# Performance work log

Measured on AMD Instinct MI355X. Metric: run time of the kernel, lower is better.

Reference implementation:

```python
import jax, jax.numpy as jnp
import numpy as np

B, L, K, S, D, H, C = 32, 256, 50, 16, 128, 4, 128
V, NN, NU, NS = 50000, 100000, 50000, 5000


def mha(q, k, v, in_w, in_b, out_w, out_b, n_heads):
    # PyTorch nn.MultiheadAttention (batch_first, eval mode) semantics.
    d = q.shape[-1]
    hd = d // n_heads
    wq, wk, wv = jnp.split(in_w, 3, axis=0)
    bq, bk, bv = jnp.split(in_b, 3)
    def heads(t):
        return t.reshape(t.shape[:-1] + (n_heads, hd))
    qh = heads(q @ wq.T + bq)
    kh = heads(k @ wk.T + bk)
    vh = heads(v @ wv.T + bv)
    scores = jnp.einsum('...qhd,...khd->...hqk', qh, kh) / jnp.sqrt(jnp.asarray(hd, q.dtype))
    attn = jax.nn.softmax(scores, axis=-1)
    o = jnp.einsum('...hqk,...khd->...qhd', attn, vh)
    o = o.reshape(o.shape[:-2] + (d,))
    return o @ out_w.T + out_b


def conv1d(x, w, b):
    # x: [B, D, L], w: [Cout, D, k]
    y = jax.lax.conv_general_dilated(x, w, (1,), 'VALID', dimension_numbers=('NCH', 'OIH', 'NCH'))
    return y + b[None, :, None]


def meta_path_module(paths, gru_wih, gru_whh, gru_bih, gru_bhh, in_w, in_b, out_w, out_b, ln_g, ln_b):
    # paths: [B, S, T, D] -> [B, D]
    b, s, t, d = paths.shape
    x = paths.reshape(b * s, t, d)
    def step(h, xt):
        gi = xt @ gru_wih.T + gru_bih
        gh = h @ gru_whh.T + gru_bhh
        ir, iz, inn = jnp.split(gi, 3, axis=-1)
        hr, hz, hn = jnp.split(gh, 3, axis=-1)
        r = jax.nn.sigmoid(ir + hr)
        z = jax.nn.sigmoid(iz + hz)
        n = jnp.tanh(inn + r * hn)
        return (1.0 - z) * n + z * h, None
    h0 = jnp.zeros((b * s, d), paths.dtype)
    h, _ = jax.lax.scan(step, h0, jnp.swapaxes(x, 0, 1))
    enc = h.reshape(b, s, d)
    attn = mha(enc, enc, enc, in_w, in_b, out_w, out_b, H)
    y = enc + attn
    mu = jnp.mean(y, -1, keepdims=True)
    var = jnp.var(y, -1, keepdims=True)
    y = (y - mu) / jnp.sqrt(var + 1e-5) * ln_g + ln_b
    return jnp.mean(y, axis=1)


def _forward(word_table, news_table, user_table, source_table,
             wa_in_w, wa_in_b, wa_out_w, wa_out_b,
             conv_w3, conv_b3, conv_w4, conv_b4, conv_w5, conv_b5, fc_w, fc_b,
             nsn_gru_wih, nsn_gru_whh, nsn_gru_bih, nsn_gru_bhh,
             nsn_in_w, nsn_in_b, nsn_out_w, nsn_out_b, nsn_ln_g, nsn_ln_b,
             nun_gru_wih, nun_gru_whh, nun_gru_bih, nun_gru_bhh,
             nun_in_w, nun_in_b, nun_out_w, nun_out_b, nun_ln_g, nun_ln_b,
             mp_w1, mp_b1, mp_w2, mp_b2, cls_w1, cls_b1, cls_w2, cls_b2,
             news_ids, news_word_indices, word_ctx_ids, nsn_src, nsn_end, nun_usr, nun_end):
    # --- fine-grained word embeds: per-token query attending over context news ---
    base = word_table[news_word_indices]              # [B, L, D]
    ctx = news_table[word_ctx_ids]                    # [B, L, K, D] (dominant gather)
    q = base[:, :, None, :]                           # [B, L, 1, D]
    fine = mha(q, ctx, ctx, wa_in_w, wa_in_b, wa_out_w, wa_out_b, H)[:, :, 0, :]
    pad = (news_word_indices == 0)[..., None]
    doc = jnp.where(pad, jnp.zeros((), base.dtype), fine)   # padding_idx=0 -> zeros
    # --- coarse CNN encoder ---
    x = jnp.swapaxes(doc, 1, 2)                       # [B, D, L]
    pooled = [jnp.max(jax.nn.relu(conv1d(x, w, b)), axis=2)
              for w, b in ((conv_w3, conv_b3), (conv_w4, conv_b4), (conv_w5, conv_b5))]
    semantic = jnp.concatenate(pooled, axis=1) @ fc_w.T + fc_b   # [B, D]
    # --- meta-path interaction ---
    start = jnp.broadcast_to(news_table[news_ids][:, None, :], (B, S, D))
    nsn_paths = jnp.stack([start, source_table[nsn_src], news_table[nsn_end]], axis=2)
    nun_paths = jnp.stack([start, user_table[nun_usr], news_table[nun_end]], axis=2)
    nsn_e = meta_path_module(nsn_paths, nsn_gru_wih, nsn_gru_whh, nsn_gru_bih, nsn_gru_bhh,
                             nsn_in_w, nsn_in_b, nsn_out_w, nsn_out_b, nsn_ln_g, nsn_ln_b)
    nun_e = meta_path_module(nun_paths, nun_gru_wih, nun_gru_whh, nun_gru_bih, nun_gru_bhh,
                             nun_in_w, nun_in_b, nun_out_w, nun_out_b, nun_ln_g, nun_ln_b)
    stack = jnp.stack([nsn_e, nun_e], axis=1)         # [B, 2, D]
    sc = jnp.tanh(stack @ mp_w1.T + mp_b1) @ mp_w2.T + mp_b2
    w = jax.nn.softmax(sc, axis=1)
    struct = jnp.sum(stack * w, axis=1)
    comb = jnp.concatenate([semantic, struct], axis=1)
    hcls = jax.nn.relu(comb @ cls_w1.T + cls_b1)
    return hcls @ cls_w2.T + cls_b2                   # [B, 2]


def setup_inputs() -> dict:
    key = jax.random.key(0)
    ks = iter(jax.random.split(key, 80))
    def p(shape):
        return (jax.random.normal(next(ks), shape, jnp.float32) * 0.02)
    inp = {}
    inp['news_ids'] = jax.random.randint(next(ks), (B,), 0, NN)
    inp['news_word_indices'] = jax.random.randint(next(ks), (B, L), 0, V)
    inp['word_ctx_ids'] = jax.random.randint(next(ks), (B, L, K), 0, NN)
    inp['nsn_src'] = jax.random.randint(next(ks), (B, S), 0, NS)
    inp['nsn_end'] = jax.random.randint(next(ks), (B, S), 0, NN)
    inp['nun_usr'] = jax.random.randint(next(ks), (B, S), 0, NU)
    inp['nun_end'] = jax.random.randint(next(ks), (B, S), 0, NN)
    inp['word_table'] = p((V, D)).at[0].set(0.0)
    inp['news_table'] = p((NN, D))
    inp['user_table'] = p((NU, D))
    inp['source_table'] = p((NS, D))
    inp['wa_in_w'] = p((3 * D, D)); inp['wa_in_b'] = p((3 * D,))
    inp['wa_out_w'] = p((D, D)); inp['wa_out_b'] = p((D,))
    for k in (3, 4, 5):
        inp[f'conv_w{k}'] = p((C, D, k)); inp[f'conv_b{k}'] = p((C,))
    inp['fc_w'] = p((D, 3 * C)); inp['fc_b'] = p((D,))
    for pre in ('nsn', 'nun'):
        inp[f'{pre}_gru_wih'] = p((3 * D, D)); inp[f'{pre}_gru_whh'] = p((3 * D, D))
        inp[f'{pre}_gru_bih'] = p((3 * D,)); inp[f'{pre}_gru_bhh'] = p((3 * D,))
        inp[f'{pre}_in_w'] = p((3 * D, D)); inp[f'{pre}_in_b'] = p((3 * D,))
        inp[f'{pre}_out_w'] = p((D, D)); inp[f'{pre}_out_b'] = p((D,))
        inp[f'{pre}_ln_g'] = jnp.ones((D,), jnp.float32); inp[f'{pre}_ln_b'] = jnp.zeros((D,), jnp.float32)
    inp['mp_w1'] = p((D // 2, D)); inp['mp_b1'] = p((D // 2,))
    inp['mp_w2'] = p((1, D // 2)); inp['mp_b2'] = p((1,))
    inp['cls_w1'] = p((D, 2 * D)); inp['cls_b1'] = p((D,))
    inp['cls_w2'] = p((2, D)); inp['cls_b2'] = p((2,))
    return inp


def reference(word_table, news_table, user_table, source_table,
              wa_in_w, wa_in_b, wa_out_w, wa_out_b,
              conv_w3, conv_b3, conv_w4, conv_b4, conv_w5, conv_b5, fc_w, fc_b,
              nsn_gru_wih, nsn_gru_whh, nsn_gru_bih, nsn_gru_bhh,
              nsn_in_w, nsn_in_b, nsn_out_w, nsn_out_b, nsn_ln_g, nsn_ln_b,
              nun_gru_wih, nun_gru_whh, nun_gru_bih, nun_gru_bhh,
              nun_in_w, nun_in_b, nun_out_w, nun_out_b, nun_ln_g, nun_ln_b,
              mp_w1, mp_b1, mp_w2, mp_b2, cls_w1, cls_b1, cls_w2, cls_b2,
              news_ids, news_word_indices, word_ctx_ids, nsn_src, nsn_end, nun_usr, nun_end):
    return _forward(word_table, news_table, user_table, source_table,
                    wa_in_w, wa_in_b, wa_out_w, wa_out_b,
                    conv_w3, conv_b3, conv_w4, conv_b4, conv_w5, conv_b5, fc_w, fc_b,
                    nsn_gru_wih, nsn_gru_whh, nsn_gru_bih, nsn_gru_bhh,
                    nsn_in_w, nsn_in_b, nsn_out_w, nsn_out_b, nsn_ln_g, nsn_ln_b,
                    nun_gru_wih, nun_gru_whh, nun_gru_bih, nun_gru_bhh,
                    nun_in_w, nun_in_b, nun_out_w, nun_out_b, nun_ln_g, nun_ln_b,
                    mp_w1, mp_b1, mp_w2, mp_b2, cls_w1, cls_b1, cls_w2, cls_b2,
                    news_ids, news_word_indices, word_ctx_ids, nsn_src, nsn_end, nun_usr, nun_end)
```

## Files before the change

kernel.cpp:

```cpp
#include <hip/hip_runtime.h>
#include <hip/hip_bf16.h>

#define BB 32
#define LL 256
#define KC 50
#define SS 16
#define DD 128
#define NH 4
#define CC 128
#define VV 50000
#define NNN 100000
#define NUU 50000
#define NSS 5000

typedef __attribute__((ext_vector_type(8))) short bf16x8;
typedef __attribute__((ext_vector_type(8))) unsigned short u16x8;
typedef __attribute__((ext_vector_type(4))) float f32x4;

#define APAD 132

__device__ __forceinline__ float dot4(float4 a, float4 b){
  return a.x*b.x + a.y*b.y + a.z*b.z + a.w*b.w;
}

__device__ __forceinline__ unsigned short f2bf(float f){
  union { float f; unsigned int u; } v; v.f = f;
  unsigned int r = (v.u + 0x7FFFu + ((v.u >> 16) & 1u)) >> 16;
  return (unsigned short)r;
}
__device__ __forceinline__ float bf2f(unsigned short s){
  union { unsigned int u; float f; } v; v.u = ((unsigned int)s) << 16;
  return v.f;
}

__global__ __launch_bounds__(256) void k_prep(
    const float* __restrict__ w3, const float* __restrict__ w4,
    const float* __restrict__ w5,
    const float* __restrict__ wih0, const float* __restrict__ whh0,
    const float* __restrict__ wih1, const float* __restrict__ whh1,
    const float* __restrict__ in_w, const float* __restrict__ out_w,
    const float* __restrict__ inw0, const float* __restrict__ outw0,
    const float* __restrict__ inw1, const float* __restrict__ outw1,
    unsigned short* __restrict__ wb3, unsigned short* __restrict__ wb4,
    unsigned short* __restrict__ wb5, unsigned short* __restrict__ wgb,
    unsigned short* __restrict__ wab, unsigned short* __restrict__ wmh){
  int e = blockIdx.x*256 + threadIdx.x;
  if (e < CC*DD*3){ int c=e/(DD*3), rm=e%(DD*3), d=rm/3, jj=rm%3;
    wb3[((size_t)jj*CC + c)*DD + d] = f2bf(w3[e]); }
  if (e < CC*DD*4){ int c=e/(DD*4), rm=e%(DD*4), d=rm/4, jj=rm%4;
    wb4[((size_t)jj*CC + c)*DD + d] = f2bf(w4[e]); }
  if (e < CC*DD*5){ int c=e/(DD*5), rm=e%(DD*5), d=rm/5, jj=rm%5;
    wb5[((size_t)jj*CC + c)*DD + d] = f2bf(w5[e]); }
  if (e < 384*DD){
    wgb[e]          = f2bf(wih0[e]);
    wgb[49152 + e]  = f2bf(whh0[e]);
    wgb[98304 + e]  = f2bf(wih1[e]);
    wgb[147456 + e] = f2bf(whh1[e]);
    wab[e]          = f2bf(in_w[e]);
  }
  if (e >= 384*DD && e < 512*DD) wab[e] = f2bf(out_w[e - 384*DD]);
  if (e < 512*DD){
    float s0 = (e < 384*DD) ? inw0[e] : outw0[e - 384*DD];
    float s1 = (e < 384*DD) ? inw1[e] : outw1[e - 384*DD];
    wmh[e]                 = f2bf(s0);
    wmh[(size_t)512*DD + e] = f2bf(s1);
  }
}

#define PST 136
#define TST 72
__global__ __launch_bounds__(256) void k_projkv(
    const float* __restrict__ news, const unsigned short* __restrict__ wkvb,
    const float* __restrict__ in_b, unsigned short* __restrict__ nK,
    unsigned short* __restrict__ nV){
  __shared__ __align__(16) unsigned short As[80*PST];
  __shared__ __align__(16) unsigned short Tw[4*16*TST];
  const int tid  = threadIdx.x;
  const int wave = tid >> 6;
  const int lane = tid & 63;
  const int l15  = lane & 15;
  const int quad = lane >> 4;
  const int r0   = blockIdx.x * 80;
  const int cw   = wave * 64;

  bf16x8 wfr[4][4];
  #pragma unroll
  for (int nt=0; nt<4; nt++)
    #pragma unroll
    for (int ks=0; ks<4; ks++)
      wfr[nt][ks] = *(const bf16x8*)(wkvb + (size_t)(cw + nt*16 + l15)*DD + ks*32 + quad*8);
  float4 bv[4];
  #pragma unroll
  for (int nt=0; nt<4; nt++)
    bv[nt] = *(const float4*)(in_b + 128 + cw + nt*16 + quad*4);

  for (int i = tid; i < 80*32; i += 256){
    int row = i >> 5, j = i & 31;
    float4 v = ((const float4*)(news + (size_t)(r0 + row)*DD))[j];
    unsigned short* d = As + row*PST + j*4;
    d[0]=f2bf(v.x); d[1]=f2bf(v.y); d[2]=f2bf(v.z); d[3]=f2bf(v.w);
  }
  __syncthreads();

  unsigned short* outp = (wave < 2) ? nK : nV;
  const int cwo = (wave & 1) * 64;
  unsigned short* tw = Tw + wave*16*TST;
  const int rr = lane >> 4;
  const int cc = lane & 15;

  #pragma unroll
  for (int mt=0; mt<5; mt++){
    bf16x8 afr[4];
    #pragma unroll
    for (int ks=0; ks<4; ks++)
      afr[ks] = *(const bf16x8*)(As + (mt*16 + l15)*PST + ks*32 + quad*8);
    f32x4 acc[4];
    #pragma unroll
    for (int nt=0; nt<4; nt++) acc[nt] = (f32x4){0.f,0.f,0.f,0.f};
    #pragma unroll
    for (int ks=0; ks<4; ks++)
      #pragma unroll
      for (int nt=0; nt<4; nt++)
        acc[nt] = __builtin_amdgcn_mfma_f32_16x16x32_bf16(wfr[nt][ks], afr[ks], acc[nt], 0,0,0);
    #pragma unroll
    for (int nt=0; nt<4; nt++){
      unsigned short pk[4];
      pk[0] = f2bf(acc[nt][0] + bv[nt].x);
      pk[1] = f2bf(acc[nt][1] + bv[nt].y);
      pk[2] = f2bf(acc[nt][2] + bv[nt].z);
      pk[3] = f2bf(acc[nt][3] + bv[nt].w);
      *(unsigned long long*)(tw + l15*TST + nt*16 + quad*4) = *(const unsigned long long*)pk;
    }
    const int gr0 = r0 + mt*16;
    #pragma unroll
    for (int s=0; s<4; s++){
      unsigned long long v = *(const unsigned long long*)(tw + (s*4 + rr)*TST + cc*4);
      *(unsigned long long*)(outp + (size_t)(gr0 + s*4 + rr)*DD + cwo + cc*4) = v;
    }
  }
}

__global__ __launch_bounds__(64) void k_qh(
    const float* __restrict__ word_table, const int* __restrict__ widx,
    const unsigned short* __restrict__ wqb, const float* __restrict__ in_b,
    float* __restrict__ qh){
  const int lane = threadIdx.x;
  const int l15 = lane & 15, quad = lane >> 4;
  const int p0 = blockIdx.x * 16;
  const int row = widx[p0 + l15];
  const float* src = word_table + (size_t)row*DD + quad*8;
  bf16x8 afr[4];
  #pragma unroll
  for (int ks=0; ks<4; ks++){
    float4 v0 = *(const float4*)(src + ks*32);
    float4 v1 = *(const float4*)(src + ks*32 + 4);
    bf16x8 a;
    a[0]=(short)f2bf(v0.x); a[1]=(short)f2bf(v0.y); a[2]=(short)f2bf(v0.z); a[3]=(short)f2bf(v0.w);
    a[4]=(short)f2bf(v1.x); a[5]=(short)f2bf(v1.y); a[6]=(short)f2bf(v1.z); a[7]=(short)f2bf(v1.w);
    afr[ks] = a;
  }
  #pragma unroll
  for (int nt=0; nt<8; nt++){
    const int n0 = nt*16;
    bf16x8 bfr[4];
    #pragma unroll
    for (int ks=0; ks<4; ks++)
      bfr[ks] = *(const bf16x8*)(wqb + (size_t)(n0+l15)*DD + ks*32 + quad*8);
    const float bias = in_b[n0 + l15];
    f32x4 acc = {0.f,0.f,0.f,0.f};
    #pragma unroll
    for (int ks=0; ks<4; ks++)
      acc = __builtin_amdgcn_mfma_f32_16x16x32_bf16(afr[ks], bfr[ks], acc, 0,0,0);
    #pragma unroll
    for (int r=0;r<4;r++){
      int m = quad*4 + r;
      qh[(size_t)(p0+m)*DD + n0 + l15] = acc[r] + bias;
    }
  }
}

__global__ __launch_bounds__(64) void k_attn(
    const float* __restrict__ qh, const unsigned short* __restrict__ nK,
    const unsigned short* __restrict__ nV, const int* __restrict__ ctx_ids,
    unsigned short* __restrict__ o_out){
  const int p = blockIdx.x;
  const int lane = threadIdx.x;
  const int r = lane >> 4;
  const int g = lane & 15;
  const int h = g >> 2;
  __shared__ int ids[52];
  __shared__ float sc[NH][52];
  if (lane < KC) ids[lane] = ctx_ids[(size_t)p*KC + lane];
  float qv[8];
  {
    const float4* qp = (const float4*)(qh + (size_t)p*DD + g*8);
    float4 q0 = qp[0], q1 = qp[1];
    qv[0]=q0.x; qv[1]=q0.y; qv[2]=q0.z; qv[3]=q0.w;
    qv[4]=q1.x; qv[5]=q1.y; qv[6]=q1.z; qv[7]=q1.w;
  }
  __syncthreads();
  for (int kb=0; kb<13; kb++){
    int k2 = kb*4 + r;
    int row = ids[(k2 < KC) ? k2 : 0];
    u16x8 kv = *(const u16x8*)(nK + (size_t)row*DD + g*8);
    float pr = 0.f;
    #pragma unroll
    for (int j=0;j<8;j++) pr += qv[j]*bf2f(kv[j]);
    pr += __shfl_xor(pr, 1, 64);
    pr += __shfl_xor(pr, 2, 64);
    if ((g & 3) == 0 && k2 < KC) sc[h][k2] = pr;
  }
  __syncthreads();
  {
    const int hh = lane >> 4, kc = lane & 15;
    const float scale = 0.17677669529663687f;
    float mx = -1e30f;
    #pragma unroll
    for (int q4=0;q4<4;q4++){ int k2=kc+q4*16; if (k2<KC) mx = fmaxf(mx, sc[hh][k2]); }
    mx = fmaxf(mx, __shfl_xor(mx, 1, 64));
    mx = fmaxf(mx, __shfl_xor(mx, 2, 64));
    mx = fmaxf(mx, __shfl_xor(mx, 4, 64));
    mx = fmaxf(mx, __shfl_xor(mx, 8, 64));
    float sm = 0.f;
    float ev[4];
    #pragma unroll
    for (int q4=0;q4<4;q4++){
      int k2=kc+q4*16;
      ev[q4] = (k2<KC) ? __expf((sc[hh][k2]-mx)*scale) : 0.f;
      sm += ev[q4];
    }
    sm += __shfl_xor(sm, 1, 64);
    sm += __shfl_xor(sm, 2, 64);
    sm += __shfl_xor(sm, 4, 64);
    sm += __shfl_xor(sm, 8, 64);
    float inv = 1.f/sm;
    #pragma unroll
    for (int q4=0;q4<4;q4++){ int k2=kc+q4*16; if (k2<KC) sc[hh][k2] = ev[q4]*inv; }
  }
  __syncthreads();
  float acc[8];
  #pragma unroll
  for (int j=0;j<8;j++) acc[j]=0.f;
  for (int kb=0; kb<13; kb++){
    int k2 = kb*4 + r;
    int row = ids[(k2 < KC) ? k2 : 0];
    float w = (k2 < KC) ? sc[h][k2] : 0.f;
    u16x8 vv = *(const u16x8*)(nV + (size_t)row*DD + g*8);
    #pragma unroll
    for (int j=0;j<8;j++) acc[j] += w*bf2f(vv[j]);
  }
  #pragma unroll
  for (int j=0;j<8;j++){
    acc[j] += __shfl_xor(acc[j], 16, 64);
    acc[j] += __shfl_xor(acc[j], 32, 64);
  }
  if (r == 0){
    u16x8 o;
    #pragma unroll
    for (int j=0;j<8;j++) o[j] = f2bf(acc[j]);
    *(u16x8*)(o_out + (size_t)p*DD + g*8) = o;
  }
}

__global__ __launch_bounds__(64) void k_wo(
    const unsigned short* __restrict__ o_attn, const int* __restrict__ widx,
    const unsigned short* __restrict__ wob, const float* __restrict__ out_b,
    unsigned short* __restrict__ doc){
  const int lane = threadIdx.x;
  const int l15 = lane & 15, quad = lane >> 4;
  const int p0 = blockIdx.x * 16;
  bf16x8 afr[4];
  #pragma unroll
  for (int ks=0; ks<4; ks++)
    afr[ks] = *(const bf16x8*)(o_attn + (size_t)(p0+l15)*DD + ks*32 + quad*8);
  int msk[4];
  #pragma unroll
  for (int r=0;r<4;r++) msk[r] = widx[p0 + quad*4 + r];
  #pragma unroll
  for (int nt=0; nt<8; nt++){
    const int n0 = nt*16;
    bf16x8 bfr[4];
    #pragma unroll
    for (int ks=0; ks<4; ks++)
      bfr[ks] = *(const bf16x8*)(wob + (size_t)(n0+l15)*DD + ks*32 + quad*8);
    const float bias = out_b[n0 + l15];
    f32x4 acc = {0.f,0.f,0.f,0.f};
    #pragma unroll
    for (int ks=0; ks<4; ks++)
      acc = __builtin_amdgcn_mfma_f32_16x16x32_bf16(afr[ks], bfr[ks], acc, 0,0,0);
    #pragma unroll
    for (int r=0;r<4;r++){
      int m = quad*4 + r;
      doc[(size_t)(p0+m)*DD + n0 + l15] = (msk[r] == 0) ? (unsigned short)0
                                                        : f2bf(acc[r] + bias);
    }
  }
}

#define CROWS 68
#define CPAD 136
__global__ __launch_bounds__(256) void k_conv(
    const unsigned short* __restrict__ doc, const unsigned short* __restrict__ wb3,
    const unsigned short* __restrict__ wb4, const unsigned short* __restrict__ wb5,
    float* __restrict__ convp){
  __shared__ __align__(16) char smem[CROWS*CPAD*2];
  unsigned short* ds = (unsigned short*)smem;
  float* smf = (float*)smem;
  const int blk = blockIdx.x;
  const int chunk = blk & 3;
  const int j = (blk >> 2) % 3;
  const int b = blk / 12;
  const int kk = 3 + j;
  const int T = LL - kk + 1;
  const int t0 = chunk * 64;
  const int nrows = 64 + kk - 1;
  const unsigned short* wb = (j==0) ? wb3 : (j==1) ? wb4 : wb5;
  const int tid = threadIdx.x;
  for (int i = tid; i < nrows*16; i += 256){
    int row = i >> 4, q8 = i & 15;
    int gt = t0 + row;
    u16x8 v = (u16x8){0,0,0,0,0,0,0,0};
    if (gt < LL) v = *(const u16x8*)(doc + ((size_t)b*LL + gt)*DD + q8*8);
    *(u16x8*)(ds + row*CPAD + q8*8) = v;
  }
  __syncthreads();
  const int wave = tid >> 6;
  const int lane = tid & 63;
  const int l15  = lane & 15;
  const int quad = lane >> 4;
  f32x4 acc[8];
  #pragma unroll
  for (int nt=0;nt<8;nt++) acc[nt] = (f32x4){0.f,0.f,0.f,0.f};
  for (int jj=0; jj<kk; jj++){
    #pragma unroll
    for (int ks=0; ks<4; ks++){
      bf16x8 af = *(const bf16x8*)(ds + (wave*16 + l15 + jj)*CPAD + ks*32 + quad*8);
      #pragma unroll
      for (int nt=0; nt<8; nt++){
        bf16x8 bf = *(const bf16x8*)(wb + ((size_t)jj*CC + nt*16 + l15)*DD + ks*32 + quad*8);
        acc[nt] = __builtin_amdgcn_mfma_f32_16x16x32_bf16(af, bf, acc[nt], 0,0,0);
      }
    }
  }
  __syncthreads();
  #pragma unroll
  for (int nt=0; nt<8; nt++){
    float mx = -1e30f;
    #pragma unroll
    for (int r=0;r<4;r++){
      int t = t0 + wave*16 + quad*4 + r;
      mx = fmaxf(mx, (t < T) ? acc[nt][r] : -1e30f);
    }
    mx = fmaxf(mx, __shfl_xor(mx, 16, 64));
    mx = fmaxf(mx, __shfl_xor(mx, 32, 64));
    if (quad == 0) smf[wave*128 + nt*16 + l15] = mx;
  }
  __syncthreads();
  if (tid < 128){
    float m4 = fmaxf(fmaxf(smf[tid], smf[128+tid]), fmaxf(smf[256+tid], smf[384+tid]));
    convp[(((size_t)b*3 + j)*4 + chunk)*CC + tid] = m4;
  }
}

#define GSTR 392
__global__ __launch_bounds__(256) void k_gru(
    const float* __restrict__ news_table, const float* __restrict__ user_table,
    const float* __restrict__ source_table,
    const int* __restrict__ news_ids, const int* __restrict__ nsn_src,
    const int* __restrict__ nsn_end, const int* __restrict__ nun_usr,
    const int* __restrict__ nun_end,
    const unsigned short* __restrict__ wgb,
    const float* __restrict__ bih0, const float* __restrict__ bhh0,
    const float* __restrict__ bih1, const float* __restrict__ bhh1,
    float* __restrict__ enc){
  __shared__ __align__(16) unsigned short xs[16][CPAD];
  __shared__ __align__(16) unsigned short hs[16][CPAD];
  __shared__ float hf[8][128];
  __shared__ float gi[8][GSTR];
  __shared__ float gh[8][GSTR];
  const int blk = blockIdx.x;
  const int m  = blk >> 6;
  const int b  = (blk >> 1) & 31;
  const int s0 = (blk & 1) * 8;
  const int tid = threadIdx.x;
  const int wave = tid >> 6, lane = tid & 63, l15 = lane & 15, quad = lane >> 4;
  const unsigned short* Wih = wgb + (size_t)m*2*384*DD;
  const unsigned short* Whh = Wih + 384*DD;
  const float* bih = m ? bih1 : bih0;
  const float* bhh = m ? bhh1 : bhh0;
  for (int i=tid;i<16*CPAD;i+=256){ (&xs[0][0])[i]=0; (&hs[0][0])[i]=0; }
  for (int i=tid;i<8*128;i+=256) (&hf[0][0])[i]=0.f;
  __syncthreads();
  for (int t=0;t<3;t++){
    {
      int s = tid >> 5, j = tid & 31;
      int row; const float* tab;
      if (t==0){ row = news_ids[b]; tab = news_table; }
      else if (t==1){ row = m ? nun_usr[b*SS+s0+s] : nsn_src[b*SS+s0+s];
                      tab = m ? user_table : source_table; }
      else { row = m ? nun_end[b*SS+s0+s] : nsn_end[b*SS+s0+s]; tab = news_table; }
      float4 v = ((const float4*)(tab + (size_t)row*DD))[j];
      unsigned short* dp = &xs[s][j*4];
      dp[0]=f2bf(v.x); dp[1]=f2bf(v.y); dp[2]=f2bf(v.z); dp[3]=f2bf(v.w);
    }
    __syncthreads();
    bf16x8 ax[4], ah[4];
    #pragma unroll
    for (int ks=0;ks<4;ks++){
      ax[ks] = *(const bf16x8*)&xs[l15][ks*32+quad*8];
      ah[ks] = *(const bf16x8*)&hs[l15][ks*32+quad*8];
    }
    #pragma unroll
    for (int nt=0;nt<6;nt++){
      const int n0 = wave*96 + nt*16;
      f32x4 ga = {0.f,0.f,0.f,0.f}, ha = {0.f,0.f,0.f,0.f};
      #pragma unroll
      for (int ks=0;ks<4;ks++){
        bf16x8 bi = *(const bf16x8*)(Wih + (size_t)(n0+l15)*DD + ks*32+quad*8);
        ga = __builtin_amdgcn_mfma_f32_16x16x32_bf16(ax[ks], bi, ga, 0,0,0);
        bf16x8 bh = *(const bf16x8*)(Whh + (size_t)(n0+l15)*DD + ks*32+quad*8);
        ha = __builtin_amdgcn_mfma_f32_16x16x32_bf16(ah[ks], bh, ha, 0,0,0);
      }
      if (quad < 2){
        #pragma unroll
        for (int r=0;r<4;r++){
          gi[quad*4+r][n0+l15] = ga[r];
          gh[quad*4+r][n0+l15] = ha[r];
        }
      }
    }
    __syncthreads();
    #pragma unroll
    for (int k=0;k<4;k++){
      int it = tid + k*256;
      int s = it >> 7, g = it & 127;
      float rr = 1.f/(1.f+__expf(-(gi[s][g] + gh[s][g] + bih[g] + bhh[g])));
      float zz = 1.f/(1.f+__expf(-(gi[s][128+g] + gh[s][128+g] + bih[128+g] + bhh[128+g])));
      float nn = tanhf(gi[s][256+g] + bih[256+g] + rr*(gh[s][256+g] + bhh[256+g]));
      float hnew = (1.f-zz)*nn + zz*hf[s][g];
      hf[s][g] = hnew;
      hs[s][g] = f2bf(hnew);
    }
    __syncthreads();
  }
  {
    int s = tid >> 5, j = tid & 31;
    float4 v = ((const float4*)hf[s])[j];
    ((float4*)(enc + (((size_t)m*BB + b)*SS + (s0+s))*DD))[j] = v;
  }
}

#define MPAD 136
__global__ __launch_bounds__(256) void k_metamha(
    const float* __restrict__ enc,
    const unsigned short* __restrict__ wmh,
    const float* __restrict__ inb0, const float* __restrict__ outb0,
    const float* __restrict__ lng0, const float* __restrict__ lnb0,
    const float* __restrict__ inb1, const float* __restrict__ outb1,
    const float* __restrict__ lng1, const float* __restrict__ lnb1,
    float* __restrict__ meta_e){
  const int m = blockIdx.x >> 5;
  const int b = blockIdx.x & 31;
  const int tid = threadIdx.x;
  const int wave = tid >> 6, lane = tid & 63, l15 = lane & 15, quad = lane >> 4;
  const unsigned short* W = wmh + (size_t)m*512*DD;
  const float* in_b  = m ? inb1 : inb0;
  const float* out_b = m ? outb1 : outb0;
  const float* lng   = m ? lng1 : lng0;
  const float* lnb   = m ? lnb1 : lnb0;

  __shared__ __align__(16) unsigned short ebf[16][MPAD];
  __shared__ __align__(16) unsigned short qb[16][MPAD];
  __shared__ __align__(16) unsigned short kb[16][MPAD];
  __shared__ __align__(16) unsigned short ob[16][MPAD];
  __shared__ float vf[16][128];
  __shared__ float er[16][132];
  __shared__ float at[NH][16][16];
  __shared__ float mu[16], rs[16];
  __shared__ float part[2][128];

  const float* esrc = enc + ((size_t)m*BB + b)*SS*DD;
  for (int i = tid; i < 16*32; i += 256){
    int s = i >> 5, j = i & 31;
    float4 v = ((const float4*)esrc)[i];
    ((float4*)er[s])[j] = v;
    unsigned short* dp = &ebf[s][j*4];
    dp[0]=f2bf(v.x); dp[1]=f2bf(v.y); dp[2]=f2bf(v.z); dp[3]=f2bf(v.w);
  }
  __syncthreads();
  {
    bf16x8 ax[4];
    #pragma unroll
    for (int ks=0;ks<4;ks++) ax[ks] = *(const bf16x8*)&ebf[l15][ks*32+quad*8];
    #pragma unroll
    for (int nt=0; nt<6; nt++){
      const int n0 = wave*96 + nt*16;
      f32x4 acc = {0.f,0.f,0.f,0.f};
      #pragma unroll
      for (int ks=0;ks<4;ks++){
        bf16x8 bw = *(const bf16x8*)(W + (size_t)(n0+l15)*DD + ks*32+quad*8);
        acc = __builtin_amdgcn_mfma_f32_16x16x32_bf16(ax[ks], bw, acc, 0,0,0);
      }
      const float bias = in_b[n0+l15];
      const int col = n0 + l15;
      #pragma unroll
      for (int r=0;r<4;r++){
        int row = quad*4+r;
        float val = acc[r] + bias;
        if (n0 < 128)      qb[row][col]       = f2bf(val);
        else if (n0 < 256) kb[row][col-128]   = f2bf(val);
        else               vf[row][col-256]   = val;
      }
    }
  }
  __syncthreads();
  {
    const int h = wave;
    bf16x8 aq = *(const bf16x8*)&qb[l15][h*32 + quad*8];
    bf16x8 ak = *(const bf16x8*)&kb[l15][h*32 + quad*8];
    f32x4 z = {0.f,0.f,0.f,0.f};
    f32x4 acc = __builtin_amdgcn_mfma_f32_16x16x32_bf16(aq, ak, z, 0,0,0);
    #pragma unroll
    for (int r=0;r<4;r++)
      at[h][quad*4+r][l15] = acc[r] * 0.17677669529663687f;
  }
  __syncthreads();
  if (tid < 64){
    int h = tid>>4, qi = tid&15;
    float mx=-1e30f;
    #pragma unroll
    for (int ki=0;ki<16;ki++) mx = fmaxf(mx, at[h][qi][ki]);
    float sm=0.f;
    float ee[16];
    #pragma unroll
    for (int ki=0;ki<16;ki++){ ee[ki]=__expf(at[h][qi][ki]-mx); sm+=ee[ki]; }
    float inv=1.f/sm;
    #pragma unroll
    for (int ki=0;ki<16;ki++) at[h][qi][ki]=ee[ki]*inv;
  }
  __syncthreads();
  {
    int c = tid & 127, h = c >> 5;
    int sBase = (tid >> 7) * 8;
    #pragma unroll
    for (int s=0;s<8;s++){
      float acc=0.f;
      #pragma unroll
      for (int ki=0;ki<16;ki++) acc += at[h][sBase+s][ki]*vf[ki][c];
      ob[sBase+s][c] = f2bf(acc);
    }
  }
  __syncthreads();
  {
    bf16x8 ao[4];
    #pragma unroll
    for (int ks=0;ks<4;ks++) ao[ks] = *(const bf16x8*)&ob[l15][ks*32+quad*8];
    #pragma unroll
    for (int nt=0; nt<2; nt++){
      const int n0 = wave*32 + nt*16;
      f32x4 acc = {0.f,0.f,0.f,0.f};
      #pragma unroll
      for (int ks=0;ks<4;ks++){
        bf16x8 bw = *(const bf16x8*)(W + (size_t)(384 + n0+l15)*DD + ks*32+quad*8);
        acc = __builtin_amdgcn_mfma_f32_16x16x32_bf16(ao[ks], bw, acc, 0,0,0);
      }
      const float bias = out_b[n0+l15];
      const int col = n0 + l15;
      #pragma unroll
      for (int r=0;r<4;r++){
        int row = quad*4 + r;
        er[row][col] += acc[r] + bias;
      }
    }
  }
  __syncthreads();
  {
    int row = tid >> 4, i = tid & 15;
    const float* yr = &er[row][i*8];
    float s1=0.f, s2=0.f;
    #pragma unroll
    for (int j2=0;j2<8;j2++){ float y=yr[j2]; s1+=y; s2+=y*y; }
    #pragma unroll
    for (int msk=1; msk<16; msk<<=1){
      s1 += __shfl_xor(s1, msk, 64);
      s2 += __shfl_xor(s2, msk, 64);
    }
    if (i==0){
      float mean = s1*(1.f/128.f);
      mu[row]=mean;
      rs[row]=rsqrtf(s2*(1.f/128.f) - mean*mean + 1e-5f);
    }
  }
  __syncthreads();
  {
    int c = tid & 127, half = tid >> 7;
    float g = lng[c], bb2 = lnb[c];
    float acc=0.f;
    #pragma unroll
    for (int s=0;s<8;s++){
      int ss = half*8+s;
      acc += (er[ss][c]-mu[ss])*rs[ss]*g + bb2;
    }
    part[half][c]=acc;
  }
  __syncthreads();
  if (tid < 128)
    meta_e[((size_t)m*BB+b)*DD + tid] = (part[0][tid]+part[1][tid]) * (1.f/16.f);
}

__global__ __launch_bounds__(128) void k_final(
    const float* __restrict__ convp,
    const float* __restrict__ cb3, const float* __restrict__ cb4,
    const float* __restrict__ cb5,
    const float* __restrict__ fc_w, const float* __restrict__ fc_b,
    const float* __restrict__ meta_e,
    const float* __restrict__ mp_w1, const float* __restrict__ mp_b1,
    const float* __restrict__ mp_w2, const float* __restrict__ mp_b2,
    const float* __restrict__ cls_w1, const float* __restrict__ cls_b1,
    const float* __restrict__ cls_w2, const float* __restrict__ cls_b2,
    float* __restrict__ out){
  const int b = blockIdx.x;
  const int c = threadIdx.x;
  __shared__ float pooled[384];
  __shared__ float comb[256];
  __shared__ float hcls[128];
  __shared__ float tt[2][64];
  __shared__ float wsc[2];
  for (int idx=c; idx<384; idx+=128){
    int j = idx >> 7, cc2 = idx & 127;
    const float* base = convp + (((size_t)b*3 + j)*4)*CC + cc2;
    float mx = -1e30f;
    for (int ci=0;ci<4;ci++) mx = fmaxf(mx, base[ci*CC]);
    const float* cb = (j==0)?cb3:(j==1)?cb4:cb5;
    pooled[idx] = fmaxf(mx + cb[cc2], 0.f);
  }
  __syncthreads();
  {
    float acc = fc_b[c];
    const float* wr = fc_w + (size_t)c*384;
    for (int i=0;i<384;i++) acc += pooled[i]*wr[i];
    comb[c] = acc;
  }
  if (c < 64){
    for (int m=0;m<2;m++){
      const float* ev = meta_e + ((size_t)m*BB+b)*DD;
      float acc = mp_b1[c];
      const float* wr = mp_w1 + (size_t)c*DD;
      for (int i=0;i<DD;i++) acc += ev[i]*wr[i];
      tt[m][c] = tanhf(acc);
    }
  }
  __syncthreads();
  if (c == 0){
    float s0 = mp_b2[0], s1 = mp_b2[0];
    for (int j=0;j<64;j++){ s0 += tt[0][j]*mp_w2[j]; s1 += tt[1][j]*mp_w2[j]; }
    float mx = fmaxf(s0,s1);
    float e0 = __expf(s0-mx), e1 = __expf(s1-mx);
    wsc[0] = e0/(e0+e1); wsc[1] = e1/(e0+e1);
  }
  __syncthreads();
  comb[128+c] = wsc[0]*meta_e[((size_t)b)*DD + c]
              + wsc[1]*meta_e[((size_t)(BB+b))*DD + c];
  __syncthreads();
  {
    float acc = cls_b1[c];
    const float* wr = cls_w1 + (size_t)c*256;
    for (int i=0;i<256;i++) acc += comb[i]*wr[i];
    hcls[c] = fmaxf(acc, 0.f);
  }
  __syncthreads();
  if (c < 2){
    float acc = cls_b2[c];
    const float* wr = cls_w2 + (size_t)c*DD;
    for (int i=0;i<DD;i++) acc += hcls[i]*wr[i];
    out[b*2 + c] = acc;
  }
}

extern "C" void kernel_launch(void* const* d_in, const int* in_sizes, int n_in,
                              void* d_out, int out_size, void* d_ws, size_t ws_size,
                              hipStream_t stream){
  const int* news_ids = (const int*)d_in[0];
  const int* nwi      = (const int*)d_in[1];
  const int* ctx_ids  = (const int*)d_in[2];
  const int* nsn_src  = (const int*)d_in[3];
  const int* nsn_end  = (const int*)d_in[4];
  const int* nun_usr  = (const int*)d_in[5];
  const int* nun_end  = (const int*)d_in[6];
  const float* word_table   = (const float*)d_in[7];
  const float* news_table   = (const float*)d_in[8];
  const float* user_table   = (const float*)d_in[9];
  const float* source_table = (const float*)d_in[10];
  const float* wa_in_w  = (const float*)d_in[11];
  const float* wa_in_b  = (const float*)d_in[12];
  const float* wa_out_w = (const float*)d_in[13];
  const float* wa_out_b = (const float*)d_in[14];
  const float* conv_w3 = (const float*)d_in[15];
  const float* conv_b3 = (const float*)d_in[16];
  const float* conv_w4 = (const float*)d_in[17];
  const float* conv_b4 = (const float*)d_in[18];
  const float* conv_w5 = (const float*)d_in[19];
  const float* conv_b5 = (const float*)d_in[20];
  const float* fc_w = (const float*)d_in[21];
  const float* fc_b = (const float*)d_in[22];
  const float* wih0 = (const float*)d_in[23];
  const float* whh0 = (const float*)d_in[24];
  const float* bih0 = (const float*)d_in[25];
  const float* bhh0 = (const float*)d_in[26];
  const float* inw0 = (const float*)d_in[27];
  const float* inb0 = (const float*)d_in[28];
  const float* outw0 = (const float*)d_in[29];
  const float* outb0 = (const float*)d_in[30];
  const float* lng0 = (const float*)d_in[31];
  const float* lnb0 = (const float*)d_in[32];
  const float* wih1 = (const float*)d_in[33];
  const float* whh1 = (const float*)d_in[34];
  const float* bih1 = (const float*)d_in[35];
  const float* bhh1 = (const float*)d_in[36];
  const float* inw1 = (const float*)d_in[37];
  const float* inb1 = (const float*)d_in[38];
  const float* outw1 = (const float*)d_in[39];
  const float* outb1 = (const float*)d_in[40];
  const float* lng1 = (const float*)d_in[41];
  const float* lnb1 = (const float*)d_in[42];
  const float* mp_w1 = (const float*)d_in[43];
  const float* mp_b1 = (const float*)d_in[44];
  const float* mp_w2 = (const float*)d_in[45];
  const float* mp_b2 = (const float*)d_in[46];
  const float* cls_w1 = (const float*)d_in[47];
  const float* cls_b1 = (const float*)d_in[48];
  const float* cls_w2 = (const float*)d_in[49];
  const float* cls_b2 = (const float*)d_in[50];

  char* wsb = (char*)d_ws;
  unsigned short* nK = (unsigned short*)wsb;
  unsigned short* nV = nK + (size_t)NNN*DD;
  unsigned short* wb3 = nV + (size_t)NNN*DD;
  unsigned short* wb4 = wb3 + (size_t)CC*DD*3;
  unsigned short* wb5 = wb4 + (size_t)CC*DD*4;
  unsigned short* wgb = wb5 + (size_t)CC*DD*5;
  unsigned short* wab = wgb + (size_t)4*384*DD;
  unsigned short* wmh = wab + (size_t)512*DD;
  float* qh     = (float*)(wmh + (size_t)2*512*DD);
  unsigned short* o_at = (unsigned short*)(qh + (size_t)BB*LL*DD);
  unsigned short* doc  = (unsigned short*)((float*)o_at + (size_t)BB*LL*DD);
  float* convp  = (float*)doc + (size_t)BB*LL*DD;
  float* enc    = convp + BB*3*4*CC;
  float* meta_e = enc + (size_t)2*BB*SS*DD;
  const size_t need_bytes = (size_t)((char*)(meta_e + 2*BB*DD) - wsb);
  if (ws_size < need_bytes) return;

  const unsigned short* wqb  = wab;
  const unsigned short* wkvb = wab + (size_t)128*DD;
  const unsigned short* wob  = wab + (size_t)384*DD;

  k_prep<<<dim3(320), dim3(256), 0, stream>>>(conv_w3, conv_w4, conv_w5,
      wih0, whh0, wih1, whh1, wa_in_w, wa_out_w,
      inw0, outw0, inw1, outw1,
      wb3, wb4, wb5, wgb, wab, wmh);
  k_projkv<<<dim3(NNN/80), dim3(256), 0, stream>>>(news_table, wkvb, wa_in_b, nK, nV);
  k_qh<<<dim3(BB*LL/16), dim3(64), 0, stream>>>(word_table, nwi, wqb, wa_in_b, qh);
  k_attn<<<dim3(BB*LL), dim3(64), 0, stream>>>(qh, nK, nV, ctx_ids, o_at);
  k_wo<<<dim3(BB*LL/16), dim3(64), 0, stream>>>(o_at, nwi, wob, wa_out_b, doc);
  k_conv<<<dim3(BB*3*4), dim3(256), 0, stream>>>(doc, wb3, wb4, wb5, convp);
  k_gru<<<dim3(128), dim3(256), 0, stream>>>(news_table, user_table, source_table,
      news_ids, nsn_src, nsn_end, nun_usr, nun_end,
      wgb, bih0, bhh0, bih1, bhh1, enc);
  k_metamha<<<dim3(64), dim3(256), 0, stream>>>(enc, wmh,
      inb0, outb0, lng0, lnb0,
      inb1, outb1, lng1, lnb1, meta_e);
  k_final<<<dim3(BB), dim3(128), 0, stream>>>(convp, conv_b3, conv_b4, conv_b5,
      fc_w, fc_b, meta_e, mp_w1, mp_b1, mp_w2, mp_b2,
      cls_w1, cls_b1, cls_w2, cls_b2, (float*)d_out);
}
```

Before: 359.0 us.

## Merge independent kernels into horizontally fused launches to cut launch count

New measurement: 360.2 us. Within noise of the previous version (+0.3%).

```diff
diff --git a/kernel.cpp b/kernel.cpp
--- a/kernel.cpp
+++ b/kernel.cpp
@@ -16,8 +16,6 @@
 typedef __attribute__((ext_vector_type(8))) short bf16x8;
 typedef __attribute__((ext_vector_type(8))) unsigned short u16x8;
 typedef __attribute__((ext_vector_type(4))) float f32x4;
-
-#define APAD 132
 
 __device__ __forceinline__ float dot4(float4 a, float4 b){
   return a.x*b.x + a.y*b.y + a.z*b.z + a.w*b.w;
@@ -67,114 +65,191 @@
   }
 }
 
+#define F1_GRU 128
+#define F1_PKV 1250
 #define PST 136
 #define TST 72
-__global__ __launch_bounds__(256) void k_projkv(
+#define CPAD 136
+#define GSTR 392
+__global__ __launch_bounds__(256) void k_fused1(
     const float* __restrict__ news, const unsigned short* __restrict__ wkvb,
-    const float* __restrict__ in_b, unsigned short* __restrict__ nK,
-    unsigned short* __restrict__ nV){
-  __shared__ __align__(16) unsigned short As[80*PST];
-  __shared__ __align__(16) unsigned short Tw[4*16*TST];
-  const int tid  = threadIdx.x;
-  const int wave = tid >> 6;
-  const int lane = tid & 63;
-  const int l15  = lane & 15;
-  const int quad = lane >> 4;
-  const int r0   = blockIdx.x * 80;
-  const int cw   = wave * 64;
-
-  bf16x8 wfr[4][4];
-  #pragma unroll
-  for (int nt=0; nt<4; nt++)
-    #pragma unroll
-    for (int ks=0; ks<4; ks++)
-      wfr[nt][ks] = *(const bf16x8*)(wkvb + (size_t)(cw + nt*16 + l15)*DD + ks*32 + quad*8);
-  float4 bv[4];
-  #pragma unroll
-  for (int nt=0; nt<4; nt++)
-    bv[nt] = *(const float4*)(in_b + 128 + cw + nt*16 + quad*4);
-
-  for (int i = tid; i < 80*32; i += 256){
-    int row = i >> 5, j = i & 31;
-    float4 v = ((const float4*)(news + (size_t)(r0 + row)*DD))[j];
-    unsigned short* d = As + row*PST + j*4;
-    d[0]=f2bf(v.x); d[1]=f2bf(v.y); d[2]=f2bf(v.z); d[3]=f2bf(v.w);
-  }
-  __syncthreads();
-
-  unsigned short* outp = (wave < 2) ? nK : nV;
-  const int cwo = (wave & 1) * 64;
-  unsigned short* tw = Tw + wave*16*TST;
-  const int rr = lane >> 4;
-  const int cc = lane & 15;
-
-  #pragma unroll
-  for (int mt=0; mt<5; mt++){
+    const float* __restrict__ in_b,
+    unsigned short* __restrict__ nK, unsigned short* __restrict__ nV,
+    const float* __restrict__ word_table, const int* __restrict__ widx,
+    const unsigned short* __restrict__ wqb, float* __restrict__ qh_out,
+    const float* __restrict__ user_table, const float* __restrict__ source_table,
+    const int* __restrict__ news_ids, const int* __restrict__ nsn_src,
+    const int* __restrict__ nsn_end, const int* __restrict__ nun_usr,
+    const int* __restrict__ nun_end, const unsigned short* __restrict__ wgb,
+    const float* __restrict__ bih0, const float* __restrict__ bhh0,
+    const float* __restrict__ bih1, const float* __restrict__ bhh1,
+    float* __restrict__ enc){
+  __shared__ __align__(16) char smem[38912];
+  const int blk = blockIdx.x;
+  const int tid = threadIdx.x;
+  const int wave = tid >> 6, lane = tid & 63, l15 = lane & 15, quad = lane >> 4;
+
+  if (blk < F1_GRU){
+    auto xs = (unsigned short(*)[CPAD])(smem);
+    auto hs = (unsigned short(*)[CPAD])(smem + 4352);
+    auto hf = (float(*)[128])(smem + 8704);
+    auto gi = (float(*)[GSTR])(smem + 12800);
+    auto gh = (float(*)[GSTR])(smem + 25344);
+    const int m  = blk >> 6;
+    const int b  = (blk >> 1) & 31;
+    const int s0 = (blk & 1) * 8;
+    const unsigned short* Wih = wgb + (size_t)m*2*384*DD;
+    const unsigned short* Whh = Wih + 384*DD;
+    const float* bih = m ? bih1 : bih0;
+    const float* bhh = m ? bhh1 : bhh0;
+    for (int i=tid;i<16*CPAD;i+=256){ (&xs[0][0])[i]=0; (&hs[0][0])[i]=0; }
+    for (int i=tid;i<8*128;i+=256) (&hf[0][0])[i]=0.f;
+    __syncthreads();
+    for (int t=0;t<3;t++){
+      {
+        int s = tid >> 5, j = tid & 31;
+        int row; const float* tab;
+        if (t==0){ row = news_ids[b]; tab = news; }
+        else if (t==1){ row = m ? nun_usr[b*SS+s0+s] : nsn_src[b*SS+s0+s];
+                        tab = m ? user_table : source_table; }
+        else { row = m ? nun_end[b*SS+s0+s] : nsn_end[b*SS+s0+s]; tab = news; }
+        float4 v = ((const float4*)(tab + (size_t)row*DD))[j];
+        unsigned short* dp = &xs[s][j*4];
+        dp[0]=f2bf(v.x); dp[1]=f2bf(v.y); dp[2]=f2bf(v.z); dp[3]=f2bf(v.w);
+      }
+      __syncthreads();
+      bf16x8 ax[4], ah[4];
+      #pragma unroll
+      for (int ks=0;ks<4;ks++){
+        ax[ks] = *(const bf16x8*)&xs[l15][ks*32+quad*8];
+        ah[ks] = *(const bf16x8*)&hs[l15][ks*32+quad*8];
+      }
+      #pragma unroll
+      for (int nt=0;nt<6;nt++){
+        const int n0 = wave*96 + nt*16;
+        f32x4 ga = {0.f,0.f,0.f,0.f}, ha = {0.f,0.f,0.f,0.f};
+        #pragma unroll
+        for (int ks=0;ks<4;ks++){
+          bf16x8 bi = *(const bf16x8*)(Wih + (size_t)(n0+l15)*DD + ks*32+quad*8);
+          ga = __builtin_amdgcn_mfma_f32_16x16x32_bf16(ax[ks], bi, ga, 0,0,0);
+          bf16x8 bh = *(const bf16x8*)(Whh + (size_t)(n0+l15)*DD + ks*32+quad*8);
+          ha = __builtin_amdgcn_mfma_f32_16x16x32_bf16(ah[ks], bh, ha, 0,0,0);
+        }
+        if (quad < 2){
+          #pragma unroll
+          for (int r=0;r<4;r++){
+            gi[quad*4+r][n0+l15] = ga[r];
+            gh[quad*4+r][n0+l15] = ha[r];
+          }
+        }
+      }
+      __syncthreads();
+      #pragma unroll
+      for (int k=0;k<4;k++){
+        int it = tid + k*256;
+        int s = it >> 7, g = it & 127;
+        float rr = 1.f/(1.f+__expf(-(gi[s][g] + gh[s][g] + bih[g] + bhh[g])));
+        float zz = 1.f/(1.f+__expf(-(gi[s][128+g] + gh[s][128+g] + bih[128+g] + bhh[128+g])));
+        float nn = tanhf(gi[s][256+g] + bih[256+g] + rr*(gh[s][256+g] + bhh[256+g]));
+        float hnew = (1.f-zz)*nn + zz*hf[s][g];
+        hf[s][g] = hnew;
+        hs[s][g] = f2bf(hnew);
+      }
+      __syncthreads();
+    }
+    {
+      int s = tid >> 5, j = tid & 31;
+      float4 v = ((const float4*)hf[s])[j];
+      ((float4*)(enc + (((size_t)m*BB + b)*SS + (s0+s))*DD))[j] = v;
+    }
+  } else if (blk < F1_GRU + F1_PKV){
+    unsigned short* As = (unsigned short*)smem;
+    unsigned short* Tw = (unsigned short*)(smem + 21760);
+    const int r0 = (blk - F1_GRU) * 80;
+    const int cw = wave * 64;
+    bf16x8 wfr[4][4];
+    #pragma unroll
+    for (int nt=0; nt<4; nt++)
+      #pragma unroll
+      for (int ks=0; ks<4; ks++)
+        wfr[nt][ks] = *(const bf16x8*)(wkvb + (size_t)(cw + nt*16 + l15)*DD + ks*32 + quad*8);
+    float4 bv[4];
+    #pragma unroll
+    for (int nt=0; nt<4; nt++)
+      bv[nt] = *(const float4*)(in_b + 128 + cw + nt*16 + quad*4);
+    for (int i = tid; i < 80*32; i += 256){
+      int row = i >> 5, j = i & 31;
+      float4 v = ((const float4*)(news + (size_t)(r0 + row)*DD))[j];
+      unsigned short* d = As + row*PST + j*4;
+      d[0]=f2bf(v.x); d[1]=f2bf(v.y); d[2]=f2bf(v.z); d[3]=f2bf(v.w);
+    }
+    __syncthreads();
+    unsigned short* outp = (wave < 2) ? nK : nV;
+    const int cwo = (wave & 1) * 64;
+    unsigned short* tw = Tw + wave*16*TST;
+    const int rr = lane >> 4;
+    const int cc = lane & 15;
+    #pragma unroll
+    for (int mt=0; mt<5; mt++){
+      bf16x8 afr[4];
+      #pragma unroll
+      for (int ks=0; ks<4; ks++)
+        afr[ks] = *(const bf16x8*)(As + (mt*16 + l15)*PST + ks*32 + quad*8);
+      f32x4 acc[4];
+      #pragma unroll
+      for (int nt=0; nt<4; nt++) acc[nt] = (f32x4){0.f,0.f,0.f,0.f};
+      #pragma unroll
+      for (int ks=0; ks<4; ks++)
+        #pragma unroll
+        for (int nt=0; nt<4; nt++)
+          acc[nt] = __builtin_amdgcn_mfma_f32_16x16x32_bf16(wfr[nt][ks], afr[ks], acc[nt], 0,0,0);
+      #pragma unroll
+      for (int nt=0; nt<4; nt++){
+        unsigned short pk[4];
+        pk[0] = f2bf(acc[nt][0] + bv[nt].x);
+        pk[1] = f2bf(acc[nt][1] + bv[nt].y);
+        pk[2] = f2bf(acc[nt][2] + bv[nt].z);
+        pk[3] = f2bf(acc[nt][3] + bv[nt].w);
+        *(unsigned long long*)(tw + l15*TST + nt*16 + quad*4) = *(const unsigned long long*)pk;
+      }
+      const int gr0 = r0 + mt*16;
+      #pragma unroll
+      for (int s=0; s<4; s++){
+        unsigned long long v = *(const unsigned long long*)(tw + (s*4 + rr)*TST + cc*4);
+        *(unsigned long long*)(outp + (size_t)(gr0 + s*4 + rr)*DD + cwo + cc*4) = v;
+      }
+    }
+  } else {
+    const int p0 = ((blk - F1_GRU - F1_PKV)*4 + wave) * 16;
+    const int row = widx[p0 + l15];
+    const float* src = word_table + (size_t)row*DD + quad*8;
     bf16x8 afr[4];
     #pragma unroll
-    for (int ks=0; ks<4; ks++)
-      afr[ks] = *(const bf16x8*)(As + (mt*16 + l15)*PST + ks*32 + quad*8);
-    f32x4 acc[4];
-    #pragma unroll
-    for (int nt=0; nt<4; nt++) acc[nt] = (f32x4){0.f,0.f,0.f,0.f};
-    #pragma unroll
-    for (int ks=0; ks<4; ks++)
-      #pragma unroll
-      for (int nt=0; nt<4; nt++)
-        acc[nt] = __builtin_amdgcn_mfma_f32_16x16x32_bf16(wfr[nt][ks], afr[ks], acc[nt], 0,0,0);
-    #pragma unroll
-    for (int nt=0; nt<4; nt++){
-      unsigned short pk[4];
-      pk[0] = f2bf(acc[nt][0] + bv[nt].x);
-      pk[1] = f2bf(acc[nt][1] + bv[nt].y);
-      pk[2] = f2bf(acc[nt][2] + bv[nt].z);
-      pk[3] = f2bf(acc[nt][3] + bv[nt].w);
-      *(unsigned long long*)(tw + l15*TST + nt*16 + quad*4) = *(const unsigned long long*)pk;
-    }
-    const int gr0 = r0 + mt*16;
-    #pragma unroll
-    for (int s=0; s<4; s++){
-      unsigned long long v = *(const unsigned long long*)(tw + (s*4 + rr)*TST + cc*4);
-      *(unsigned long long*)(outp + (size_t)(gr0 + s*4 + rr)*DD + cwo + cc*4) = v;
-    }
-  }
-}
-
-__global__ __launch_bounds__(64) void k_qh(
-    const float* __restrict__ word_table, const int* __restrict__ widx,
-    const unsigned short* __restrict__ wqb, const float* __restrict__ in_b,
-    float* __restrict__ qh){
-  const int lane = threadIdx.x;
-  const int l15 = lane & 15, quad = lane >> 4;
-  const int p0 = blockIdx.x * 16;
-  const int row = widx[p0 + l15];
-  const float* src = word_table + (size_t)row*DD + quad*8;
-  bf16x8 afr[4];
-  #pragma unroll
-  for (int ks=0; ks<4; ks++){
-    float4 v0 = *(const float4*)(src + ks*32);
-    float4 v1 = *(const float4*)(src + ks*32 + 4);
-    bf16x8 a;
-    a[0]=(short)f2bf(v0.x); a[1]=(short)f2bf(v0.y); a[2]=(short)f2bf(v0.z); a[3]=(short)f2bf(v0.w);
-    a[4]=(short)f2bf(v1.x); a[5]=(short)f2bf(v1.y); a[6]=(short)f2bf(v1.z); a[7]=(short)f2bf(v1.w);
-    afr[ks] = a;
-  }
-  #pragma unroll
-  for (int nt=0; nt<8; nt++){
-    const int n0 = nt*16;
-    bf16x8 bfr[4];
-    #pragma unroll
-    for (int ks=0; ks<4; ks++)
-      bfr[ks] = *(const bf16x8*)(wqb + (size_t)(n0+l15)*DD + ks*32 + quad*8);
-    const float bias = in_b[n0 + l15];
-    f32x4 acc = {0.f,0.f,0.f,0.f};
-    #pragma unroll
-    for (int ks=0; ks<4; ks++)
-      acc = __builtin_amdgcn_mfma_f32_16x16x32_bf16(afr[ks], bfr[ks], acc, 0,0,0);
-    #pragma unroll
-    for (int r=0;r<4;r++){
-      int m = quad*4 + r;
-      qh[(size_t)(p0+m)*DD + n0 + l15] = acc[r] + bias;
+    for (int ks=0; ks<4; ks++){
+      float4 v0 = *(const float4*)(src + ks*32);
+      float4 v1 = *(const float4*)(src + ks*32 + 4);
+      bf16x8 a;
+      a[0]=(short)f2bf(v0.x); a[1]=(short)f2bf(v0.y); a[2]=(short)f2bf(v0.z); a[3]=(short)f2bf(v0.w);
+      a[4]=(short)f2bf(v1.x); a[5]=(short)f2bf(v1.y); a[6]=(short)f2bf(v1.z); a[7]=(short)f2bf(v1.w);
+      afr[ks] = a;
+    }
+    #pragma unroll
+    for (int nt=0; nt<8; nt++){
+      const int n0 = nt*16;
+      bf16x8 bfr[4];
+      #pragma unroll
+      for (int ks=0; ks<4; ks++)
+        bfr[ks] = *(const bf16x8*)(wqb + (size_t)(n0+l15)*DD + ks*32 + quad*8);
+      const float bias = in_b[n0 + l15];
+      f32x4 acc = {0.f,0.f,0.f,0.f};
+      #pragma unroll
+      for (int ks=0; ks<4; ks++)
+        acc = __builtin_amdgcn_mfma_f32_16x16x32_bf16(afr[ks], bfr[ks], acc, 0,0,0);
+      #pragma unroll
+      for (int r=0;r<4;r++){
+        int m = quad*4 + r;
+        qh_out[(size_t)(p0+m)*DD + n0 + l15] = acc[r] + bias;
+      }
     }
   }
 }
@@ -262,43 +337,200 @@
   }
 }
 
-__global__ __launch_bounds__(64) void k_wo(
+#define MPAD 136
+__global__ __launch_bounds__(256) void k_fused2(
     const unsigned short* __restrict__ o_attn, const int* __restrict__ widx,
     const unsigned short* __restrict__ wob, const float* __restrict__ out_b,
-    unsigned short* __restrict__ doc){
-  const int lane = threadIdx.x;
-  const int l15 = lane & 15, quad = lane >> 4;
-  const int p0 = blockIdx.x * 16;
-  bf16x8 afr[4];
-  #pragma unroll
-  for (int ks=0; ks<4; ks++)
-    afr[ks] = *(const bf16x8*)(o_attn + (size_t)(p0+l15)*DD + ks*32 + quad*8);
-  int msk[4];
-  #pragma unroll
-  for (int r=0;r<4;r++) msk[r] = widx[p0 + quad*4 + r];
-  #pragma unroll
-  for (int nt=0; nt<8; nt++){
-    const int n0 = nt*16;
-    bf16x8 bfr[4];
+    unsigned short* __restrict__ doc,
+    const float* __restrict__ enc, const unsigned short* __restrict__ wmh,
+    const float* __restrict__ inb0, const float* __restrict__ outb0,
+    const float* __restrict__ lng0, const float* __restrict__ lnb0,
+    const float* __restrict__ inb1, const float* __restrict__ outb1,
+    const float* __restrict__ lng1, const float* __restrict__ lnb1,
+    float* __restrict__ meta_e){
+  __shared__ __align__(16) char smem[39296];
+  const int blk = blockIdx.x;
+  const int tid = threadIdx.x;
+  const int wave = tid >> 6, lane = tid & 63, l15 = lane & 15, quad = lane >> 4;
+
+  if (blk < 128){
+    const int p0 = (blk*4 + wave) * 16;
+    bf16x8 afr[4];
     #pragma unroll
     for (int ks=0; ks<4; ks++)
-      bfr[ks] = *(const bf16x8*)(wob + (size_t)(n0+l15)*DD + ks*32 + quad*8);
-    const float bias = out_b[n0 + l15];
-    f32x4 acc = {0.f,0.f,0.f,0.f};
-    #pragma unroll
-    for (int ks=0; ks<4; ks++)
-      acc = __builtin_amdgcn_mfma_f32_16x16x32_bf16(afr[ks], bfr[ks], acc, 0,0,0);
-    #pragma unroll
-    for (int r=0;r<4;r++){
-      int m = quad*4 + r;
-      doc[(size_t)(p0+m)*DD + n0 + l15] = (msk[r] == 0) ? (unsigned short)0
-                                                        : f2bf(acc[r] + bias);
-    }
+      afr[ks] = *(const bf16x8*)(o_attn + (size_t)(p0+l15)*DD + ks*32 + quad*8);
+    int msk[4];
+    #pragma unroll
+    for (int r=0;r<4;r++) msk[r] = widx[p0 + quad*4 + r];
+    #pragma unroll
+    for (int nt=0; nt<8; nt++){
+      const int n0 = nt*16;
+      bf16x8 bfr[4];
+      #pragma unroll
+      for (int ks=0; ks<4; ks++)
+        bfr[ks] = *(const bf16x8*)(wob + (size_t)(n0+l15)*DD + ks*32 + quad*8);
+      const float bias = out_b[n0 + l15];
+      f32x4 acc = {0.f,0.f,0.f,0.f};
+      #pragma unroll
+      for (int ks=0; ks<4; ks++)
+        acc = __builtin_amdgcn_mfma_f32_16x16x32_bf16(afr[ks], bfr[ks], acc, 0,0,0);
+      #pragma unroll
+      for (int r=0;r<4;r++){
+        int m = quad*4 + r;
+        doc[(size_t)(p0+m)*DD + n0 + l15] = (msk[r] == 0) ? (unsigned short)0
+                                                          : f2bf(acc[r] + bias);
+      }
+    }
+  } else {
+    auto ebf = (unsigned short(*)[MPAD])(smem);
+    auto qb  = (unsigned short(*)[MPAD])(smem + 4352);
+    auto kb  = (unsigned short(*)[MPAD])(smem + 8704);
+    auto ob  = (unsigned short(*)[MPAD])(smem + 13056);
+    auto vf  = (float(*)[128])(smem + 17408);
+    auto er  = (float(*)[132])(smem + 25600);
+    auto at  = (float(*)[16][16])(smem + 34048);
+    float* mu = (float*)(smem + 38144);
+    float* rs = (float*)(smem + 38208);
+    auto part = (float(*)[128])(smem + 38272);
+    const int mb = blk - 128;
+    const int m = mb >> 5;
+    const int b = mb & 31;
+    const unsigned short* W = wmh + (size_t)m*512*DD;
+    const float* in_b  = m ? inb1 : inb0;
+    const float* outb  = m ? outb1 : outb0;
+    const float* lng   = m ? lng1 : lng0;
+    const float* lnb   = m ? lnb1 : lnb0;
+    const float* esrc = enc + ((size_t)m*BB + b)*SS*DD;
+    for (int i = tid; i < 16*32; i += 256){
+      int s = i >> 5, j = i & 31;
+      float4 v = ((const float4*)esrc)[i];
+      ((float4*)er[s])[j] = v;
+      unsigned short* dp = &ebf[s][j*4];
+      dp[0]=f2bf(v.x); dp[1]=f2bf(v.y); dp[2]=f2bf(v.z); dp[3]=f2bf(v.w);
+    }
+    __syncthreads();
+    {
+      bf16x8 ax[4];
+      #pragma unroll
+      for (int ks=0;ks<4;ks++) ax[ks] = *(const bf16x8*)&ebf[l15][ks*32+quad*8];
+      #pragma unroll
+      for (int nt=0; nt<6; nt++){
+        const int n0 = wave*96 + nt*16;
+        f32x4 acc = {0.f,0.f,0.f,0.f};
+        #pragma unroll
+        for (int ks=0;ks<4;ks++){
+          bf16x8 bw = *(const bf16x8*)(W + (size_t)(n0+l15)*DD + ks*32+quad*8);
+          acc = __builtin_amdgcn_mfma_f32_16x16x32_bf16(ax[ks], bw, acc, 0,0,0);
+        }
+        const float bias = in_b[n0+l15];
+        const int col = n0 + l15;
+        #pragma unroll
+        for (int r=0;r<4;r++){
+          int row = quad*4+r;
+          float val = acc[r] + bias;
+          if (n0 < 128)      qb[row][col]       = f2bf(val);
+          else if (n0 < 256) kb[row][col-128]   = f2bf(val);
+          else               vf[row][col-256]   = val;
+        }
+      }
+    }
+    __syncthreads();
+    {
+      const int h = wave;
+      bf16x8 aq = *(const bf16x8*)&qb[l15][h*32 + quad*8];
+      bf16x8 ak = *(const bf16x8*)&kb[l15][h*32 + quad*8];
+      f32x4 z = {0.f,0.f,0.f,0.f};
+      f32x4 acc = __builtin_amdgcn_mfma_f32_16x16x32_bf16(aq, ak, z, 0,0,0);
+      #pragma unroll
+      for (int r=0;r<4;r++)
+        at[h][quad*4+r][l15] = acc[r] * 0.17677669529663687f;
+    }
+    __syncthreads();
+    if (tid < 64){
+      int h = tid>>4, qi = tid&15;
+      float mx=-1e30f;
+      #pragma unroll
+      for (int ki=0;ki<16;ki++) mx = fmaxf(mx, at[h][qi][ki]);
+      float sm=0.f;
+      float ee[16];
+      #pragma unroll
+      for (int ki=0;ki<16;ki++){ ee[ki]=__expf(at[h][qi][ki]-mx); sm+=ee[ki]; }
+      float inv=1.f/sm;
+      #pragma unroll
+      for (int ki=0;ki<16;ki++) at[h][qi][ki]=ee[ki]*inv;
+    }
+    __syncthreads();
+    {
+      int c = tid & 127, h = c >> 5;
+      int sBase = (tid >> 7) * 8;
+      #pragma unroll
+      for (int s=0;s<8;s++){
+        float acc=0.f;
+        #pragma unroll
+        for (int ki=0;ki<16;ki++) acc += at[h][sBase+s][ki]*vf[ki][c];
+        ob[sBase+s][c] = f2bf(acc);
+      }
+    }
+    __syncthreads();
+    {
+      bf16x8 ao[4];
+      #pragma unroll
+      for (int ks=0;ks<4;ks++) ao[ks] = *(const bf16x8*)&ob[l15][ks*32+quad*8];
+      #pragma unroll
+      for (int nt=0; nt<2; nt++){
+        const int n0 = wave*32 + nt*16;
+        f32x4 acc = {0.f,0.f,0.f,0.f};
+        #pragma unroll
+        for (int ks=0;ks<4;ks++){
+          bf16x8 bw = *(const bf16x8*)(W + (size_t)(384 + n0+l15)*DD + ks*32+quad*8);
+          acc = __builtin_amdgcn_mfma_f32_16x16x32_bf16(ao[ks], bw, acc, 0,0,0);
+        }
+        const float bias = outb[n0+l15];
+        const int col = n0 + l15;
+        #pragma unroll
+        for (int r=0;r<4;r++){
+          int row = quad*4 + r;
+          er[row][col] += acc[r] + bias;
+        }
+      }
+    }
+    __syncthreads();
+    {
+      int row = tid >> 4, i = tid & 15;
+      const float* yr = &er[row][i*8];
+      float s1=0.f, s2=0.f;
+      #pragma unroll
+      for (int j2=0;j2<8;j2++){ float y=yr[j2]; s1+=y; s2+=y*y; }
+      #pragma unroll
+      for (int msk2=1; msk2<16; msk2<<=1){
+        s1 += __shfl_xor(s1, msk2, 64);
+        s2 += __shfl_xor(s2, msk2, 64);
+      }
+      if (i==0){
+        float mean = s1*(1.f/128.f);
+        mu[row]=mean;
+        rs[row]=rsqrtf(s2*(1.f/128.f) - mean*mean + 1e-5f);
+      }
+    }
+    __syncthreads();
+    {
+      int c = tid & 127, half = tid >> 7;
+      float g = lng[c], bb2 = lnb[c];
+      float acc=0.f;
+      #pragma unroll
+      for (int s=0;s<8;s++){
+        int ss = half*8+s;
+        acc += (er[ss][c]-mu[ss])*rs[ss]*g + bb2;
+      }
+      part[half][c]=acc;
+    }
+    __syncthreads();
+    if (tid < 128)
+      meta_e[((size_t)m*BB+b)*DD + tid] = (part[0][tid]+part[1][tid]) * (1.f/16.f);
   }
 }
 
 #define CROWS 68
-#define CPAD 136
 __global__ __launch_bounds__(256) void k_conv(
     const unsigned short* __restrict__ doc, const unsigned short* __restrict__ wb3,
     const unsigned short* __restrict__ wb4, const unsigned short* __restrict__ wb5,
@@ -360,252 +592,6 @@
     float m4 = fmaxf(fmaxf(smf[tid], smf[128+tid]), fmaxf(smf[256+tid], smf[384+tid]));
     convp[(((size_t)b*3 + j)*4 + chunk)*CC + tid] = m4;
   }
-}
-
-#define GSTR 392
-__global__ __launch_bounds__(256) void k_gru(
-    const float* __restrict__ news_table, const float* __restrict__ user_table,
-    const float* __restrict__ source_table,
-    const int* __restrict__ news_ids, const int* __restrict__ nsn_src,
-    const int* __restrict__ nsn_end, const int* __restrict__ nun_usr,
-    const int* __restrict__ nun_end,
-    const unsigned short* __restrict__ wgb,
-    const float* __restrict__ bih0, const float* __restrict__ bhh0,
-    const float* __restrict__ bih1, const float* __restrict__ bhh1,
-    float* __restrict__ enc){
-  __shared__ __align__(16) unsigned short xs[16][CPAD];
-  __shared__ __align__(16) unsigned short hs[16][CPAD];
-  __shared__ float hf[8][128];
-  __shared__ float gi[8][GSTR];
-  __shared__ float gh[8][GSTR];
-  const int blk = blockIdx.x;
-  const int m  = blk >> 6;
-  const int b  = (blk >> 1) & 31;
-  const int s0 = (blk & 1) * 8;
-  const int tid = threadIdx.x;
-  const int wave = tid >> 6, lane = tid & 63, l15 = lane & 15, quad = lane >> 4;
-  const unsigned short* Wih = wgb + (size_t)m*2*384*DD;
-  const unsigned short* Whh = Wih + 384*DD;
-  const float* bih = m ? bih1 : bih0;
-  const float* bhh = m ? bhh1 : bhh0;
-  for (int i=tid;i<16*CPAD;i+=256){ (&xs[0][0])[i]=0; (&hs[0][0])[i]=0; }
-  for (int i=tid;i<8*128;i+=256) (&hf[0][0])[i]=0.f;
-  __syncthreads();
-  for (int t=0;t<3;t++){
-    {
-      int s = tid >> 5, j = tid & 31;
-      int row; const float* tab;
-      if (t==0){ row = news_ids[b]; tab = news_table; }
-      else if (t==1){ row = m ? nun_usr[b*SS+s0+s] : nsn_src[b*SS+s0+s];
-                      tab = m ? user_table : source_table; }
-      else { row = m ? nun_end[b*SS+s0+s] : nsn_end[b*SS+s0+s]; tab = news_table; }
-      float4 v = ((const float4*)(tab + (size_t)row*DD))[j];
-      unsigned short* dp = &xs[s][j*4];
-      dp[0]=f2bf(v.x); dp[1]=f2bf(v.y); dp[2]=f2bf(v.z); dp[3]=f2bf(v.w);
-    }
-    __syncthreads();
-    bf16x8 ax[4], ah[4];
-    #pragma unroll
-    for (int ks=0;ks<4;ks++){
-      ax[ks] = *(const bf16x8*)&xs[l15][ks*32+quad*8];
-      ah[ks] = *(const bf16x8*)&hs[l15][ks*32+quad*8];
-    }
-    #pragma unroll
-    for (int nt=0;nt<6;nt++){
-      const int n0 = wave*96 + nt*16;
-      f32x4 ga = {0.f,0.f,0.f,0.f}, ha = {0.f,0.f,0.f,0.f};
-      #pragma unroll
-      for (int ks=0;ks<4;ks++){
-        bf16x8 bi = *(const bf16x8*)(Wih + (size_t)(n0+l15)*DD + ks*32+quad*8);
-        ga = __builtin_amdgcn_mfma_f32_16x16x32_bf16(ax[ks], bi, ga, 0,0,0);
-        bf16x8 bh = *(const bf16x8*)(Whh + (size_t)(n0+l15)*DD + ks*32+quad*8);
-        ha = __builtin_amdgcn_mfma_f32_16x16x32_bf16(ah[ks], bh, ha, 0,0,0);
-      }
-      if (quad < 2){
-        #pragma unroll
-        for (int r=0;r<4;r++){
-          gi[quad*4+r][n0+l15] = ga[r];
-          gh[quad*4+r][n0+l15] = ha[r];
-        }
-      }
-    }
-    __syncthreads();
-    #pragma unroll
-    for (int k=0;k<4;k++){
-      int it = tid + k*256;
-      int s = it >> 7, g = it & 127;
-      float rr = 1.f/(1.f+__expf(-(gi[s][g] + gh[s][g] + bih[g] + bhh[g])));
-      float zz = 1.f/(1.f+__expf(-(gi[s][128+g] + gh[s][128+g] + bih[128+g] + bhh[128+g])));
-      float nn = tanhf(gi[s][256+g] + bih[256+g] + rr*(gh[s][256+g] + bhh[256+g]));
-      float hnew = (1.f-zz)*nn + zz*hf[s][g];
-      hf[s][g] = hnew;
-      hs[s][g] = f2bf(hnew);
-    }
-    __syncthreads();
-  }
-  {
-    int s = tid >> 5, j = tid & 31;
-    float4 v = ((const float4*)hf[s])[j];
-    ((float4*)(enc + (((size_t)m*BB + b)*SS + (s0+s))*DD))[j] = v;
-  }
-}
-
-#define MPAD 136
-__global__ __launch_bounds__(256) void k_metamha(
-    const float* __restrict__ enc,
-    const unsigned short* __restrict__ wmh,
-    const float* __restrict__ inb0, const float* __restrict__ outb0,
-    const float* __restrict__ lng0, const float* __restrict__ lnb0,
-    const float* __restrict__ inb1, const float* __restrict__ outb1,
-    const float* __restrict__ lng1, const float* __restrict__ lnb1,
-    float* __restrict__ meta_e){
-  const int m = blockIdx.x >> 5;
-  const int b = blockIdx.x & 31;
-  const int tid = threadIdx.x;
-  const int wave = tid >> 6, lane = tid & 63, l15 = lane & 15, quad = lane >> 4;
-  const unsigned short* W = wmh + (size_t)m*512*DD;
-  const float* in_b  = m ? inb1 : inb0;
-  const float* out_b = m ? outb1 : outb0;
-  const float* lng   = m ? lng1 : lng0;
-  const float* lnb   = m ? lnb1 : lnb0;
-
-  __shared__ __align__(16) unsigned short ebf[16][MPAD];
-  __shared__ __align__(16) unsigned short qb[16][MPAD];
-  __shared__ __align__(16) unsigned short kb[16][MPAD];
-  __shared__ __align__(16) unsigned short ob[16][MPAD];
-  __shared__ float vf[16][128];
-  __shared__ float er[16][132];
-  __shared__ float at[NH][16][16];
-  __shared__ float mu[16], rs[16];
-  __shared__ float part[2][128];
-
-  const float* esrc = enc + ((size_t)m*BB + b)*SS*DD;
-  for (int i = tid; i < 16*32; i += 256){
-    int s = i >> 5, j = i & 31;
-    float4 v = ((const float4*)esrc)[i];
-    ((float4*)er[s])[j] = v;
-    unsigned short* dp = &ebf[s][j*4];
-    dp[0]=f2bf(v.x); dp[1]=f2bf(v.y); dp[2]=f2bf(v.z); dp[3]=f2bf(v.w);
-  }
-  __syncthreads();
-  {
-    bf16x8 ax[4];
-    #pragma unroll
-    for (int ks=0;ks<4;ks++) ax[ks] = *(const bf16x8*)&ebf[l15][ks*32+quad*8];
-    #pragma unroll
-    for (int nt=0; nt<6; nt++){
-      const int n0 = wave*96 + nt*16;
-      f32x4 acc = {0.f,0.f,0.f,0.f};
-      #pragma unroll
-      for (int ks=0;ks<4;ks++){
-        bf16x8 bw = *(const bf16x8*)(W + (size_t)(n0+l15)*DD + ks*32+quad*8);
-        acc = __builtin_amdgcn_mfma_f32_16x16x32_bf16(ax[ks], bw, acc, 0,0,0);
-      }
-      const float bias = in_b[n0+l15];
-      const int col = n0 + l15;
-      #pragma unroll
-      for (int r=0;r<4;r++){
-        int row = quad*4+r;
-        float val = acc[r] + bias;
-        if (n0 < 128)      qb[row][col]       = f2bf(val);
-        else if (n0 < 256) kb[row][col-128]   = f2bf(val);
-        else               vf[row][col-256]   = val;
-      }
-    }
-  }
-  __syncthreads();
-  {
-    const int h = wave;
-    bf16x8 aq = *(const bf16x8*)&qb[l15][h*32 + quad*8];
-    bf16x8 ak = *(const bf16x8*)&kb[l15][h*32 + quad*8];
-    f32x4 z = {0.f,0.f,0.f,0.f};
-    f32x4 acc = __builtin_amdgcn_mfma_f32_16x16x32_bf16(aq, ak, z, 0,0,0);
-    #pragma unroll
-    for (int r=0;r<4;r++)
-      at[h][quad*4+r][l15] = acc[r] * 0.17677669529663687f;
-  }
-  __syncthreads();
-  if (tid < 64){
-    int h = tid>>4, qi = tid&15;
-    float mx=-1e30f;
-    #pragma unroll
-    for (int ki=0;ki<16;ki++) mx = fmaxf(mx, at[h][qi][ki]);
-    float sm=0.f;
-    float ee[16];
-    #pragma unroll
-    for (int ki=0;ki<16;ki++){ ee[ki]=__expf(at[h][qi][ki]-mx); sm+=ee[ki]; }
-    float inv=1.f/sm;
-    #pragma unroll
-    for (int ki=0;ki<16;ki++) at[h][qi][ki]=ee[ki]*inv;
-  }
-  __syncthreads();
-  {
-    int c = tid & 127, h = c >> 5;
-    int sBase = (tid >> 7) * 8;
-    #pragma unroll
-    for (int s=0;s<8;s++){
-      float acc=0.f;
-      #pragma unroll
-      for (int ki=0;ki<16;ki++) acc += at[h][sBase+s][ki]*vf[ki][c];
-      ob[sBase+s][c] = f2bf(acc);
-    }
-  }
-  __syncthreads();
-  {
-    bf16x8 ao[4];
-    #pragma unroll
-    for (int ks=0;ks<4;ks++) ao[ks] = *(const bf16x8*)&ob[l15][ks*32+quad*8];
-    #pragma unroll
-    for (int nt=0; nt<2; nt++){
-      const int n0 = wave*32 + nt*16;
-      f32x4 acc = {0.f,0.f,0.f,0.f};
-      #pragma unroll
-      for (int ks=0;ks<4;ks++){
-        bf16x8 bw = *(const bf16x8*)(W + (size_t)(384 + n0+l15)*DD + ks*32+quad*8);
-        acc = __builtin_amdgcn_mfma_f32_16x16x32_bf16(ao[ks], bw, acc, 0,0,0);
-      }
-      const float bias = out_b[n0+l15];
-      const int col = n0 + l15;
-      #pragma unroll
-      for (int r=0;r<4;r++){
-        int row = quad*4 + r;
-        er[row][col] += acc[r] + bias;
-      }
-    }
-  }
-  __syncthreads();
-  {
-    int row = tid >> 4, i = tid & 15;
-    const float* yr = &er[row][i*8];
-    float s1=0.f, s2=0.f;
-    #pragma unroll
-    for (int j2=0;j2<8;j2++){ float y=yr[j2]; s1+=y; s2+=y*y; }
-    #pragma unroll
-    for (int msk=1; msk<16; msk<<=1){
-      s1 += __shfl_xor(s1, msk, 64);
-      s2 += __shfl_xor(s2, msk, 64);
-    }
-    if (i==0){
-      float mean = s1*(1.f/128.f);
-      mu[row]=mean;
-      rs[row]=rsqrtf(s2*(1.f/128.f) - mean*mean + 1e-5f);
-    }
-  }
-  __syncthreads();
-  {
-    int c = tid & 127, half = tid >> 7;
-    float g = lng[c], bb2 = lnb[c];
-    float acc=0.f;
-    #pragma unroll
-    for (int s=0;s<8;s++){
-      int ss = half*8+s;
-      acc += (er[ss][c]-mu[ss])*rs[ss]*g + bb2;
-    }
-    part[half][c]=acc;
-  }
-  __syncthreads();
-  if (tid < 128)
-    meta_e[((size_t)m*BB+b)*DD + tid] = (part[0][tid]+part[1][tid]) * (1.f/16.f);
 }
 
 __global__ __launch_bounds__(128) void k_final(
@@ -758,17 +744,15 @@
       wih0, whh0, wih1, whh1, wa_in_w, wa_out_w,
       inw0, outw0, inw1, outw1,
       wb3, wb4, wb5, wgb, wab, wmh);
-  k_projkv<<<dim3(NNN/80), dim3(256), 0, stream>>>(news_table, wkvb, wa_in_b, nK, nV);
-  k_qh<<<dim3(BB*LL/16), dim3(64), 0, stream>>>(word_table, nwi, wqb, wa_in_b, qh);
+  k_fused1<<<dim3(F1_GRU + F1_PKV + 128), dim3(256), 0, stream>>>(
+      news_table, wkvb, wa_in_b, nK, nV,
+      word_table, nwi, wqb, qh,
+      user_table, source_table, news_ids, nsn_src, nsn_end, nun_usr, nun_end,
+      wgb, bih0, bhh0, bih1, bhh1, enc);
   k_attn<<<dim3(BB*LL), dim3(64), 0, stream>>>(qh, nK, nV, ctx_ids, o_at);
-  k_wo<<<dim3(BB*LL/16), dim3(64), 0, stream>>>(o_at, nwi, wob, wa_out_b, doc);
+  k_fused2<<<dim3(192), dim3(256), 0, stream>>>(o_at, nwi, wob, wa_out_b, doc,
+      enc, wmh, inb0, outb0, lng0, lnb0, inb1, outb1, lng1, lnb1, meta_e);
   k_conv<<<dim3(BB*3*4), dim3(256), 0, stream>>>(doc, wb3, wb4, wb5, convp);
-  k_gru<<<dim3(128), dim3(256), 0, stream>>>(news_table, user_table, source_table,
-      news_ids, nsn_src, nsn_end, nun_usr, nun_end,
-      wgb, bih0, bhh0, bih1, bhh1, enc);
-  k_metamha<<<dim3(64), dim3(256), 0, stream>>>(enc, wmh,
-      inb0, outb0, lng0, lnb0,
-      inb1, outb1, lng1, lnb1, meta_e);
   k_final<<<dim3(BB), dim3(128), 0, stream>>>(convp, conv_b3, conv_b4, conv_b5,
       fc_w, fc_b, meta_e, mp_w1, mp_b1, mp_w2, mp_b2,
       cls_w1, cls_b1, cls_w2, cls_b2, (float*)d_out);
```
